# Kernel optimization log

Hardware: AMD Instinct MI355X
Metric: run time of the kernel (lower is better)

## Reference

```python
import jax, jax.numpy as jnp
import numpy as np

IN_C, HID, OUT = 3, 128, 256
K1, K2 = 16, 8
N = 8192


def _knn_idx(x, k):
    # x: [N, C] -> indices of k nearest neighbors (excluding self), [N, k]
    n = x.shape[0]
    sq = jnp.sum(x * x, axis=1)
    d = sq[:, None] + sq[None, :] - 2.0 * (x @ x.T)  # [N, N] squared dists
    i = jnp.arange(n)
    d = d.at[i, i].set(jnp.inf)  # loop=False: exclude self
    _, idx = jax.lax.top_k(-d, k)
    return idx


def _edge_conv(x, W1, b1, W2, b2, k):
    # DynamicEdgeConv: knn graph on x, edge feat [x_i, x_j - x_i], MLP, max aggr
    n, c = x.shape
    idx = _knn_idx(x, k)              # [N, k]
    xj = x[idx]                       # [N, k, C]
    xi = x[:, None, :]                # [N, 1, C]
    e = jnp.concatenate([jnp.broadcast_to(xi, (n, k, c)), xj - xi], axis=-1)  # [N, k, 2C]
    h = jax.nn.relu(e @ W1 + b1) @ W2 + b2  # [N, k, H]
    return jnp.max(h, axis=1)               # max aggregation -> [N, H]


def setup_inputs() -> dict:
    key = jax.random.key(0)
    ks = jax.random.split(key, 9)
    def lin(k, fan_in, fan_out):
        bound = 1.0 / np.sqrt(fan_in)
        kw, kb = jax.random.split(k)
        W = jax.random.uniform(kw, (fan_in, fan_out), jnp.float32, -bound, bound)
        b = jax.random.uniform(kb, (fan_out,), jnp.float32, -bound, bound)
        return W, b
    x = jax.random.normal(ks[0], (N, IN_C), jnp.float32)
    W1a, b1a = lin(ks[1], 2 * IN_C, HID)
    W1b, b1b = lin(ks[2], HID, HID)
    W2a, b2a = lin(ks[3], 2 * HID, OUT)
    W2b, b2b = lin(ks[4], OUT, OUT)
    return {"x": x, "W1a": W1a, "b1a": b1a, "W1b": W1b, "b1b": b1b,
            "W2a": W2a, "b2a": b2a, "W2b": W2b, "b2b": b2b}


def reference(x, W1a, b1a, W1b, b1b, W2a, b2a, W2b, b2b):
    h = _edge_conv(x, W1a, b1a, W1b, b1b, K1)   # [N, HID]
    out = _edge_conv(h, W2a, b2a, W2b, b2b, K2)  # [N, OUT]
    return out
```

## Files before the change

kernel.cpp:

```cpp
#include <hip/hip_runtime.h>
#include <math.h>

constexpr int NPTS  = 8192;
constexpr int HIDC  = 128;
constexpr int OUTC2 = 256;
constexpr int PQC   = 512;
constexpr int KK1   = 16;
constexpr int KK2   = 8;

typedef __attribute__((ext_vector_type(8))) short short8;
typedef __attribute__((ext_vector_type(4))) float f32x4;

__device__ __forceinline__ f32x4 mfma16(short8 a, short8 b, f32x4 c) {
  return __builtin_amdgcn_mfma_f32_16x16x32_bf16(a, b, c, 0, 0, 0);
}

__device__ __forceinline__ void async_ld16(void* lds, const void* g) {
  __builtin_amdgcn_global_load_lds(
      (const __attribute__((address_space(1))) unsigned int*)g,
      (__attribute__((address_space(3))) unsigned int*)lds, 16, 0, 0);
}

template <int K>
__device__ __forceinline__ void ins_u(unsigned (&kk)[K], unsigned v) {
  if (v < kk[K - 1]) {
    kk[K - 1] = v;
    #pragma unroll
    for (int p = K - 1; p > 0; --p) {
      unsigned a = kk[p - 1], b = kk[p];
      kk[p - 1] = a < b ? a : b;
      kk[p]     = a < b ? b : a;
    }
  }
}

template <int K>
__device__ __forceinline__ void ins_lex(float (&kf)[K], int (&ki)[K], float v, int j) {
  bool ins = (v < kf[K - 1]) || (v == kf[K - 1] && j < ki[K - 1]);
  if (ins) {
    kf[K - 1] = v; ki[K - 1] = j;
    #pragma unroll
    for (int p = K - 1; p > 0; --p) {
      float fa = kf[p - 1], fb = kf[p];
      int   ia = ki[p - 1], ib = ki[p];
      bool sw = (fb < fa) || (fb == fa && ib < ia);
      kf[p - 1] = sw ? fb : fa; ki[p - 1] = sw ? ib : ia;
      kf[p]     = sw ? fa : fb; ki[p]     = sw ? ia : ib;
    }
  }
}

__device__ __forceinline__ unsigned short bf16_rn(float x) {
  unsigned int u = __float_as_uint(x);
  unsigned int r = u + 0x7fffu + ((u >> 16) & 1u);
  return (unsigned short)(r >> 16);
}

__global__ void pack_x_kernel(const float* __restrict__ x, float4* __restrict__ x4) {
  int i = blockIdx.x * blockDim.x + threadIdx.x;
  if (i < NPTS) {
    float a = x[3 * i], b = x[3 * i + 1], c = x[3 * i + 2];
    x4[i] = make_float4(a, b, c, a * a + b * b + c * c);
  }
}

__global__ void prep_w1f_kernel(const float* __restrict__ W1,
                                unsigned short* __restrict__ WcFhi,
                                unsigned short* __restrict__ WcFlo) {
  int idx = blockIdx.x * 256 + threadIdx.x;
  int k = idx >> 9, c = idx & 511;
  float wh = W1[(size_t)(HIDC + k) * OUTC2 + (c & 255)];
  float w = (c < OUTC2) ? (W1[(size_t)k * OUTC2 + c] - wh) : wh;
  unsigned short hi = bf16_rn(w);
  float fh = __uint_as_float(((unsigned int)hi) << 16);
  unsigned short lo = bf16_rn(w - fh);
  const int nt = c >> 4, ct = c & 15;
  const int s = k >> 5, kg = (k >> 3) & 3, e = k & 7;
  const size_t fidx = ((size_t)(s * 32 + nt) * 64 + (kg * 16 + ct)) * 8 + e;
  WcFhi[fidx] = hi;
  WcFlo[fidx] = lo;
}

__global__ void prep_w1b_kernel(const float* __restrict__ W,
                                unsigned short* __restrict__ Fhi,
                                unsigned short* __restrict__ Flo) {
  const int c = blockIdx.x;
  const int k = threadIdx.x;
  float w = W[(size_t)k * HIDC + c];
  unsigned short hi = bf16_rn(w);
  float fh = __uint_as_float(((unsigned int)hi) << 16);
  unsigned short lo = bf16_rn(w - fh);
  const int nt = c >> 4, ct = c & 15;
  const int s = k >> 5, kg = (k >> 3) & 3, e = k & 7;
  const size_t idx = ((size_t)(s * 8 + nt) * 64 + (kg * 16 + ct)) * 8 + e;
  Fhi[idx] = hi;
  Flo[idx] = lo;
}

__global__ void prep_w2_kernel(const float* __restrict__ W2,
                               unsigned short* __restrict__ W2Fhi,
                               unsigned short* __restrict__ W2Flo) {
  const int c = blockIdx.x;
  const int k = threadIdx.x;
  float w = W2[(size_t)k * OUTC2 + c];
  unsigned short hi = bf16_rn(w);
  float fh = __uint_as_float(((unsigned int)hi) << 16);
  unsigned short lo = bf16_rn(w - fh);
  const int nt = c >> 4, ct = c & 15;
  const int s  = k >> 5, kg = (k >> 3) & 3, e = k & 7;
  const int lane = kg * 16 + ct;
  const size_t idx = ((size_t)(s * 16 + nt) * 64 + lane) * 8 + e;
  W2Fhi[idx] = hi;
  W2Flo[idx] = lo;
}

__global__ __launch_bounds__(256) void knn3_kernel(const float4* __restrict__ X4,
                                                   int* __restrict__ idx_out) {
  const int tid  = threadIdx.x;
  const int lane = tid & 63;
  const int wv   = __builtin_amdgcn_readfirstlane(tid >> 6);
  const int q    = blockIdx.x * 4 + wv;

  const float4 qv = X4[q];

  unsigned kk[KK2];
  #pragma unroll
  for (int k = 0; k < KK2; ++k) kk[k] = 0xFFFFFFFFu;

  for (int c = 0; c < NPTS / 64; ++c) {
    const int j = c * 64 + lane;
    float4 pj = X4[j];
    float d = fmaxf(qv.w + pj.w - 2.f * (qv.x * pj.x + qv.y * pj.y + qv.z * pj.z), 0.f);
    unsigned key = (__float_as_uint(d) & 0xFFFFE000u) | (unsigned)j;
    if (j == q) key = 0xFFFFFFFFu;
    ins_u<KK2>(kk, key);
  }

  float kf[KK2]; int kj[KK2];
  #pragma unroll
  for (int k = 0; k < KK2; ++k) { kf[k] = INFINITY; kj[k] = 0x7fffffff; }
  #pragma unroll
  for (int k = 0; k < KK2; ++k) {
    int j = (int)(kk[k] & 0x1FFFu);
    float4 pj = X4[j];
    float d = qv.w + pj.w - 2.f * (qv.x * pj.x + qv.y * pj.y + qv.z * pj.z);
    if (kk[k] == 0xFFFFFFFFu) { d = INFINITY; j = 0x7fffffff; }
    ins_lex<KK2>(kf, kj, d, j);
  }

  #pragma unroll
  for (int k = 0; k < KK1; ++k) {
    float mf = kf[0]; int mj = kj[0];
    #pragma unroll
    for (int m = 1; m <= 32; m <<= 1) {
      float of = __shfl_xor(mf, m, 64);
      int   oj = __shfl_xor(mj, m, 64);
      bool g = (of < mf) || (of == mf && oj < mj);
      mf = g ? of : mf; mj = g ? oj : mj;
    }
    const bool won = (kf[0] == mf) && (kj[0] == mj);
    if (won) {
      idx_out[(size_t)q * KK1 + k] = mj;
      #pragma unroll
      for (int p = 0; p < KK2 - 1; ++p) { kf[p] = kf[p + 1]; kj[p] = kj[p + 1]; }
      kf[KK2 - 1] = INFINITY; kj[KK2 - 1] = 0x7fffffff;
    }
  }
}

__global__ __launch_bounds__(512) void edgeconv1_kernel(
    const float* __restrict__ X, const int* __restrict__ knn,
    const float* __restrict__ W1, const float* __restrict__ b1,
    const unsigned short* __restrict__ W1bFhi, const unsigned short* __restrict__ W1bFlo,
    const float* __restrict__ b2,
    float* __restrict__ H, unsigned short* __restrict__ Hhi,
    unsigned short* __restrict__ Hlo, float* __restrict__ SQ2) {
  __shared__ __align__(16) unsigned short Ghi[128 * HIDC];
  __shared__ __align__(16) unsigned short Glo[128 * HIDC];
  __shared__ __align__(16) unsigned short Bs[2][2][4096];
  __shared__ float xjs[8][KK1][3];
  __shared__ float xis[8][3];
  const int tid  = threadIdx.x;
  const int lane = tid & 63;
  const int wv   = __builtin_amdgcn_readfirstlane(tid >> 6);
  const int p    = blockIdx.x * 8 + wv;

  if (lane < KK1) {
    int j = knn[p * KK1 + lane];
    xjs[wv][lane][0] = X[3 * j]; xjs[wv][lane][1] = X[3 * j + 1]; xjs[wv][lane][2] = X[3 * j + 2];
  } else if (lane < KK1 + 3) {
    xis[wv][lane - KK1] = X[3 * p + lane - KK1];
  }
  __syncthreads();

  {
    const int ch0 = lane * 2;
    float2 w1r[6];
    #pragma unroll
    for (int c = 0; c < 6; ++c)
      w1r[c] = make_float2(W1[c * HIDC + ch0], W1[c * HIDC + ch0 + 1]);
    const float2 b1v = make_float2(b1[ch0], b1[ch0 + 1]);
    const float xi0 = xis[wv][0], xi1 = xis[wv][1], xi2 = xis[wv][2];
    const float base0 = b1v.x + xi0 * w1r[0].x + xi1 * w1r[1].x + xi2 * w1r[2].x;
    const float base1 = b1v.y + xi0 * w1r[0].y + xi1 * w1r[1].y + xi2 * w1r[2].y;
    #pragma unroll
    for (int e = 0; e < KK1; ++e) {
      float dx = xjs[wv][e][0] - xi0, dy = xjs[wv][e][1] - xi1, dz = xjs[wv][e][2] - xi2;
      float v0 = fmaxf(base0 + dx * w1r[3].x + dy * w1r[4].x + dz * w1r[5].x, 0.f);
      float v1 = fmaxf(base1 + dx * w1r[3].y + dy * w1r[4].y + dz * w1r[5].y, 0.f);
      unsigned short h0 = bf16_rn(v0), h1s = bf16_rn(v1);
      unsigned short l0 = bf16_rn(v0 - __uint_as_float(((unsigned)h0) << 16));
      unsigned short l1 = bf16_rn(v1 - __uint_as_float(((unsigned)h1s) << 16));
      const int r   = wv * 16 + e;
      const int off = r * 256 + (((ch0 >> 3) ^ (r & 7)) << 4) + ((ch0 & 7) << 1);
      *(ushort2*)((char*)Ghi + off) = make_ushort2(h0, h1s);
      *(ushort2*)((char*)Glo + off) = make_ushort2(l0, l1);
    }
  }

  auto stageB = [&](int buf, int s) {
    const size_t go = (size_t)s * 4096 + (size_t)wv * 512 + (size_t)lane * 8;
    async_ld16((char*)&Bs[buf][0][0] + wv * 1024, W1bFhi + go);
    async_ld16((char*)&Bs[buf][1][0] + wv * 1024, W1bFlo + go);
  };

  stageB(0, 0);
  asm volatile("s_waitcnt vmcnt(0)" ::: "memory");
  __syncthreads();

  const int col = lane & 15;
  const int kg  = lane >> 4;
  const int ar  = wv * 16 + col;
  const int abase = ar * 256;

  f32x4 acc[8];
  #pragma unroll
  for (int n = 0; n < 8; ++n) acc[n] = (f32x4){0.f, 0.f, 0.f, 0.f};

  for (int s = 0; s < 4; ++s) {
    const int cur = s & 1;
    if (s + 1 < 4) stageB(cur ^ 1, s + 1);
    const int asl = (((s * 4 + kg) ^ (ar & 7)) << 4);
    short8 ghi = *(const short8*)((const char*)Ghi + abase + asl);
    short8 glo = *(const short8*)((const char*)Glo + abase + asl);
    #pragma unroll
    for (int n = 0; n < 8; ++n) {
      const int bo = (n * 64 + lane) * 16;
      short8 bhi = *(const short8*)((const char*)&Bs[cur][0][0] + bo);
      short8 blo = *(const short8*)((const char*)&Bs[cur][1][0] + bo);
      acc[n] = mfma16(ghi, bhi, acc[n]);
      acc[n] = mfma16(ghi, blo, acc[n]);
      acc[n] = mfma16(glo, bhi, acc[n]);
    }
    asm volatile("s_waitcnt vmcnt(0)" ::: "memory");
    __syncthreads();
  }

  float sq = 0.f;
  float hv[8];
  #pragma unroll
  for (int n = 0; n < 8; ++n) {
    float m = fmaxf(fmaxf(acc[n][0], acc[n][1]), fmaxf(acc[n][2], acc[n][3]));
    m = fmaxf(m, __shfl_xor(m, 16, 64));
    m = fmaxf(m, __shfl_xor(m, 32, 64));
    m += b2[n * 16 + col];
    hv[n] = m;
    sq += m * m;
  }
  if (kg == 0) {
    #pragma unroll
    for (int n = 0; n < 8; ++n) {
      const int ch = n * 16 + col;
      H[(size_t)p * HIDC + ch] = hv[n];
      unsigned short hb = bf16_rn(hv[n]);
      float fh = __uint_as_float(((unsigned)hb) << 16);
      Hhi[(size_t)p * HIDC + ch] = hb;
      Hlo[(size_t)p * HIDC + ch] = bf16_rn(hv[n] - fh);
    }
  }
  #pragma unroll
  for (int m2 = 1; m2 <= 8; m2 <<= 1) sq += __shfl_xor(sq, m2, 64);
  if (lane == 0) SQ2[p] = sq;
}

__global__ __launch_bounds__(512) void gemm_pq_kernel(
    const unsigned short* __restrict__ Hhi, const unsigned short* __restrict__ Hlo,
    const unsigned short* __restrict__ WcFhi, const unsigned short* __restrict__ WcFlo,
    const float* __restrict__ b1, float* __restrict__ PQ) {
  __shared__ __align__(16) unsigned short Ahi[64 * HIDC];
  __shared__ __align__(16) unsigned short Alo[64 * HIDC];
  __shared__ __align__(16) unsigned short Bsl[2][2][8192];
  const int tid  = threadIdx.x;
  const int lane = tid & 63;
  const int wv   = __builtin_amdgcn_readfirstlane(tid >> 6);
  const int mb   = blockIdx.x >> 1;
  const int ns   = blockIdx.x & 1;
  const int r0   = mb * 64;

  #pragma unroll
  for (int i = 0; i < 2; ++i) {
    const int srow = wv * 8 + i * 4 + (lane >> 4);
    const int sslt = (lane & 15) ^ (srow & 7);
    const size_t go = (size_t)(r0 + srow) * HIDC + sslt * 8;
    async_ld16((char*)Ahi + (wv * 8 + i * 4) * 256, Hhi + go);
    async_ld16((char*)Alo + (wv * 8 + i * 4) * 256, Hlo + go);
  }
  auto stageB = [&](int buf, int s) {
    #pragma unroll
    for (int i = 0; i < 2; ++i) {
      const size_t go = (size_t)(s * 32 + ns * 16) * 512 + (size_t)wv * 1024 + i * 512 + lane * 8;
      async_ld16((char*)&Bsl[buf][0][0] + wv * 2048 + i * 1024, WcFhi + go);
      async_ld16((char*)&Bsl[buf][1][0] + wv * 2048 + i * 1024, WcFlo + go);
    }
  };
  stageB(0, 0);
  asm volatile("s_waitcnt vmcnt(0)" ::: "memory");
  __syncthreads();

  const int col = lane & 15;
  const int kg  = lane >> 4;
  const int mt  = wv & 3;
  const int nh  = wv >> 2;
  const int ar  = mt * 16 + col;
  const int abase = ar * 256;

  f32x4 acc[8];
  #pragma unroll
  for (int n = 0; n < 8; ++n) acc[n] = (f32x4){0.f, 0.f, 0.f, 0.f};

  for (int s = 0; s < 4; ++s) {
    const int cur = s & 1;
    if (s + 1 < 4) stageB(cur ^ 1, s + 1);
    const int asl = (((s * 4 + kg) ^ (ar & 7)) << 4);
    short8 ahi8 = *(const short8*)((const char*)Ahi + abase + asl);
    short8 alo8 = *(const short8*)((const char*)Alo + abase + asl);
    #pragma unroll
    for (int n = 0; n < 8; ++n) {
      const int ntl = nh * 8 + n;
      const int bo = (ntl * 64 + lane) * 16;
      short8 bhi = *(const short8*)((const char*)&Bsl[cur][0][0] + bo);
      short8 blo = *(const short8*)((const char*)&Bsl[cur][1][0] + bo);
      acc[n] = mfma16(ahi8, bhi, acc[n]);
      acc[n] = mfma16(ahi8, blo, acc[n]);
      acc[n] = mfma16(alo8, bhi, acc[n]);
    }
    asm volatile("s_waitcnt vmcnt(0)" ::: "memory");
    __syncthreads();
  }

  #pragma unroll
  for (int n = 0; n < 8; ++n) {
    const int cg = ns * 256 + (nh * 8 + n) * 16 + col;
    const float bb = (ns == 0) ? b1[cg] : 0.f;
    #pragma unroll
    for (int r = 0; r < 4; ++r) {
      const int row = r0 + mt * 16 + kg * 4 + r;
      PQ[(size_t)row * PQC + cg] = acc[n][r] + bb;
    }
  }
}

constexpr int JSPLIT = 16;
constexpr int JPB2   = NPTS / JSPLIT;
constexpr int NCH    = JPB2 / 16;
constexpr int CPQ    = JSPLIT * KK2;

__global__ __launch_bounds__(256) void knn128_filter_kernel(
    const unsigned short* __restrict__ Hhi, const unsigned short* __restrict__ Hlo,
    const float* __restrict__ SQ, unsigned* __restrict__ pk2) {
  __shared__ __align__(16) unsigned short As[2][2][16 * HIDC];
  const int tid  = threadIdx.x;
  const int lane = tid & 63;
  const int wv   = __builtin_amdgcn_readfirstlane(tid >> 6);
  const int qb   = blockIdx.x >> 4;
  const int js   = blockIdx.x & 15;
  const int col  = lane & 15;
  const int kg   = lane >> 4;
  const int qg   = qb * 64 + wv * 16 + col;

  short8 qhi[4], qlo[4];
  #pragma unroll
  for (int s = 0; s < 4; ++s) {
    const size_t o = (size_t)qg * HIDC + s * 32 + kg * 8;
    qhi[s] = *reinterpret_cast<const short8*>(Hhi + o);
    qlo[s] = *reinterpret_cast<const short8*>(Hlo + o);
  }
  const float sqq = SQ[qg];

  unsigned kk[KK2];
  #pragma unroll
  for (int k = 0; k < KK2; ++k) kk[k] = 0xFFFFFFFFu;

  const int jbase = js * JPB2;

  const int srow = 4 * wv + (lane >> 4);
  const int sslt = (lane & 15) ^ (srow & 7);
  auto stage = [&](int buf, int ch) {
    const size_t gofs = (size_t)(jbase + ch * 16 + srow) * HIDC + sslt * 8;
    async_ld16((char*)&As[buf][0][0] + wv * 1024, Hhi + gofs);
    async_ld16((char*)&As[buf][1][0] + wv * 1024, Hlo + gofs);
  };

  stage(0, 0);
  asm volatile("s_waitcnt vmcnt(0)" ::: "memory");
  __syncthreads();

  for (int ch = 0; ch < NCH; ++ch) {
    const int cur = ch & 1;
    if (ch + 1 < NCH) stage(cur ^ 1, ch + 1);

    const int jb = jbase + ch * 16;
    short8 ahi[4], alo[4];
    const int rowb = col * 256;
    #pragma unroll
    for (int s = 0; s < 4; ++s) {
      const int sl = ((s * 4 + kg) ^ (col & 7)) * 16;
      ahi[s] = *(const short8*)((const char*)&As[cur][0][0] + rowb + sl);
      alo[s] = *(const short8*)((const char*)&As[cur][1][0] + rowb + sl);
    }
    f32x4 sqjv = *reinterpret_cast<const f32x4*>(SQ + jb + kg * 4);

    f32x4 acc = {0.f, 0.f, 0.f, 0.f};
    #pragma unroll
    for (int s = 0; s < 4; ++s) {
      acc = mfma16(ahi[s], qhi[s], acc);
      acc = mfma16(ahi[s], qlo[s], acc);
      acc = mfma16(alo[s], qhi[s], acc);
    }
    #pragma unroll
    for (int r = 0; r < 4; ++r) {
      const int jg = jb + kg * 4 + r;
      float d = fmaxf(sqq + sqjv[r] - 2.f * acc[r], 0.f);
      unsigned key = (__float_as_uint(d) & 0xFFFFE000u) | (unsigned)jg;
      if (jg == qg) key = 0xFFFFFFFFu;
      ins_u<KK2>(kk, key);
    }
    asm volatile("s_waitcnt vmcnt(0)" ::: "memory");
    __syncthreads();
  }

  #pragma unroll
  for (int dlt = 16; dlt <= 32; dlt <<= 1) {
    unsigned ok[KK2];
    #pragma unroll
    for (int k = 0; k < KK2; ++k) ok[k] = __shfl_xor((int)kk[k], dlt, 64);
    #pragma unroll
    for (int k = 0; k < KK2; ++k) ins_u<KK2>(kk, ok[k]);
  }
  if (lane < 16) {
    const size_t base = (size_t)qg * CPQ + js * KK2;
    #pragma unroll
    for (int k = 0; k < KK2; ++k) pk2[base + k] = kk[k];
  }
}

__global__ __launch_bounds__(256) void knn_rescore_kernel(
    const float* __restrict__ H, const float* __restrict__ SQ,
    const unsigned* __restrict__ pk2, int* __restrict__ idx_out) {
  __shared__ float qrow[16][HIDC + 4];
  const int tid  = threadIdx.x;
  const int lane = tid & 63;
  const int wv   = tid >> 6;
  const int g    = lane >> 4;
  const int sl   = lane & 15;
  const int q0   = blockIdx.x * 16;
  const int qloc = wv * 4 + g;
  const int q    = q0 + qloc;

  for (int u = tid; u < 16 * 32; u += 256) {
    int r = u >> 5, c4 = u & 31;
    *(f32x4*)&qrow[r][c4 * 4] = *(const f32x4*)&H[(size_t)(q0 + r) * HIDC + c4 * 4];
  }
  __syncthreads();

  unsigned kreg[KK2];
  {
    const unsigned* src = pk2 + (size_t)q * CPQ + sl * KK2;
    uint4 a = *(const uint4*)(src);
    uint4 b = *(const uint4*)(src + 4);
    kreg[0] = a.x; kreg[1] = a.y; kreg[2] = a.z; kreg[3] = a.w;
    kreg[4] = b.x; kreg[5] = b.y; kreg[6] = b.z; kreg[7] = b.w;
  }

  unsigned ckey = 0xFFFFFFFFu;
  #pragma unroll
  for (int t = 0; t < 16; ++t) {
    unsigned m = kreg[0];
    #pragma unroll
    for (int mm = 1; mm <= 8; mm <<= 1) {
      unsigned o = (unsigned)__shfl_xor((int)m, mm, 64);
      m = o < m ? o : m;
    }
    if (t == sl) ckey = m;
    const bool won = (kreg[0] == m);
    if (won) {
      #pragma unroll
      for (int p = 0; p < KK2 - 1; ++p) kreg[p] = kreg[p + 1];
      kreg[KK2 - 1] = 0xFFFFFFFFu;
    }
  }
  const int ci = (int)(ckey & 0x1FFFu);

  const float* crow = H + (size_t)ci * HIDC;
  float dot = 0.f;
  #pragma unroll 8
  for (int c4 = 0; c4 < HIDC / 4; ++c4) {
    f32x4 qv = *(const f32x4*)&qrow[qloc][c4 * 4];
    f32x4 cv = *(const f32x4*)(crow + c4 * 4);
    dot += qv[0] * cv[0] + qv[1] * cv[1] + qv[2] * cv[2] + qv[3] * cv[3];
  }
  float d = SQ[q] + SQ[ci] - 2.f * dot;

  float kf[KK2]; int ki[KK2];
  kf[0] = d; ki[0] = ci;
  #pragma unroll
  for (int k = 1; k < KK2; ++k) { kf[k] = INFINITY; ki[k] = 0x7fffffff; }
  #pragma unroll
  for (int dlt = 1; dlt <= 8; dlt <<= 1) {
    float of[KK2]; int oi[KK2];
    #pragma unroll
    for (int k = 0; k < KK2; ++k) { of[k] = __shfl_xor(kf[k], dlt, 64); oi[k] = __shfl_xor(ki[k], dlt, 64); }
    #pragma unroll
    for (int k = 0; k < KK2; ++k) ins_lex<KK2>(kf, ki, of[k], oi[k]);
  }
  if (sl == 0) {
    #pragma unroll
    for (int k = 0; k < KK2; ++k) idx_out[(size_t)q * KK2 + k] = ki[k];
  }
}

__global__ __launch_bounds__(512) void edgeconv2_kernel(
    const float* __restrict__ PQ, const int* __restrict__ knn,
    const unsigned short* __restrict__ W2Fhi, const unsigned short* __restrict__ W2Flo,
    const float* __restrict__ b2, float* __restrict__ Out) {
  __shared__ __align__(16) unsigned short Ghi[64 * OUTC2];
  __shared__ __align__(16) unsigned short Glo[64 * OUTC2];
  __shared__ __align__(16) unsigned short Bs[2][2][8192];
  const int tid  = threadIdx.x;
  const int lane = tid & 63;
  const int wv   = __builtin_amdgcn_readfirstlane(tid >> 6);
  const int p_base = blockIdx.x * 8;

  {
    const int p   = p_base + wv;
    const int ch0 = lane * 4;
    f32x4 pv = *(const f32x4*)&PQ[(size_t)p * PQC + ch0];
    #pragma unroll
    for (int e = 0; e < KK2; ++e) {
      const int j = knn[p * KK2 + e];
      f32x4 qv = *(const f32x4*)&PQ[(size_t)j * PQC + OUTC2 + ch0];
      unsigned short hb[4], lb[4];
      #pragma unroll
      for (int c = 0; c < 4; ++c) {
        float g = fmaxf(pv[c] + qv[c], 0.f);
        hb[c] = bf16_rn(g);
        float fh = __uint_as_float(((unsigned int)hb[c]) << 16);
        lb[c] = bf16_rn(g - fh);
      }
      const int r   = wv * 8 + e;
      const int off = r * 512 + (((ch0 >> 3) ^ (r & 7)) << 4) + ((ch0 & 7) << 1);
      *(ushort4*)((char*)Ghi + off) = make_ushort4(hb[0], hb[1], hb[2], hb[3]);
      *(ushort4*)((char*)Glo + off) = make_ushort4(lb[0], lb[1], lb[2], lb[3]);
    }
  }

  auto stageB = [&](int buf, int s) {
    #pragma unroll
    for (int i = 0; i < 2; ++i) {
      const size_t go = (size_t)s * 8192 + (size_t)(wv * 2 + i) * 512 + (size_t)lane * 8;
      async_ld16((char*)&Bs[buf][0][0] + (wv * 2 + i) * 1024, W2Fhi + go);
      async_ld16((char*)&Bs[buf][1][0] + (wv * 2 + i) * 1024, W2Flo + go);
    }
  };

  stageB(0, 0);
  asm volatile("s_waitcnt vmcnt(0)" ::: "memory");
  __syncthreads();

  const int col = lane & 15;
  const int kg  = lane >> 4;
  const int mt  = wv & 3;
  const int nh  = wv >> 2;
  const int ar  = mt * 16 + col;
  const int abase = ar * 512;

  f32x4 acc[8];
  #pragma unroll
  for (int n = 0; n < 8; ++n) acc[n] = (f32x4){0.f, 0.f, 0.f, 0.f};

  for (int s = 0; s < 8; ++s) {
    const int cur = s & 1;
    if (s + 1 < 8) stageB(cur ^ 1, s + 1);

    const int asl = (((s * 4 + kg) ^ (ar & 7)) << 4);
    short8 ghi = *(const short8*)((const char*)Ghi + abase + asl);
    short8 glo = *(const short8*)((const char*)Glo + abase + asl);
    #pragma unroll
    for (int n = 0; n < 8; ++n) {
      const int nt = nh * 8 + n;
      const int bo = (nt * 64 + lane) * 16;
      short8 bhi = *(const short8*)((const char*)&Bs[cur][0][0] + bo);
      short8 blo = *(const short8*)((const char*)&Bs[cur][1][0] + bo);
      acc[n] = mfma16(ghi, bhi, acc[n]);
      acc[n] = mfma16(ghi, blo, acc[n]);
      acc[n] = mfma16(glo, bhi, acc[n]);
    }
    asm volatile("s_waitcnt vmcnt(0)" ::: "memory");
    __syncthreads();
  }

  const int pt = p_base + mt * 2 + (kg >> 1);
  #pragma unroll
  for (int n = 0; n < 8; ++n) {
    float m = fmaxf(fmaxf(acc[n][0], acc[n][1]), fmaxf(acc[n][2], acc[n][3]));
    m = fmaxf(m, __shfl_xor(m, 16, 64));
    if ((kg & 1) == 0) {
      const int ncol = nh * 128 + n * 16 + col;
      Out[(size_t)pt * OUTC2 + ncol] = m + b2[ncol];
    }
  }
}

extern "C" void kernel_launch(void* const* d_in, const int* in_sizes, int n_in,
                              void* d_out, int out_size, void* d_ws, size_t ws_size,
                              hipStream_t stream) {
  const float* x   = (const float*)d_in[0];
  const float* W1a = (const float*)d_in[1];
  const float* b1a = (const float*)d_in[2];
  const float* W1b = (const float*)d_in[3];
  const float* b1b = (const float*)d_in[4];
  const float* W2a = (const float*)d_in[5];
  const float* b2a = (const float*)d_in[6];
  const float* W2b = (const float*)d_in[7];
  const float* b2b = (const float*)d_in[8];
  float* out = (float*)d_out;

  float* h    = (float*)d_ws;
  float* sq2  = h + (size_t)NPTS * HIDC;
  int*   idx1 = (int*)(sq2 + NPTS);
  int*   idx2 = idx1 + (size_t)NPTS * KK1;
  unsigned short* Hhi = (unsigned short*)(idx2 + (size_t)NPTS * KK2);
  unsigned short* Hlo = Hhi + (size_t)NPTS * HIDC;
  unsigned* pk2 = (unsigned*)(Hlo + (size_t)NPTS * HIDC);
  float* PQ   = (float*)(pk2 + (size_t)NPTS * CPQ);
  unsigned short* W2Fhi = (unsigned short*)(PQ + (size_t)NPTS * PQC);
  unsigned short* W2Flo = W2Fhi + (size_t)OUTC2 * OUTC2;
  unsigned short* WcFhi = W2Flo + (size_t)OUTC2 * OUTC2;
  unsigned short* WcFlo = WcFhi + (size_t)HIDC * PQC;
  unsigned short* W1bFhi = WcFlo + (size_t)HIDC * PQC;
  unsigned short* W1bFlo = W1bFhi + (size_t)HIDC * HIDC;
  float4* x4 = (float4*)h;

  pack_x_kernel<<<(NPTS + 255) / 256, 256, 0, stream>>>(x, x4);
  prep_w1f_kernel<<<(HIDC * PQC) / 256, 256, 0, stream>>>(W2a, WcFhi, WcFlo);
  prep_w1b_kernel<<<HIDC, HIDC, 0, stream>>>(W1b, W1bFhi, W1bFlo);
  prep_w2_kernel<<<OUTC2, OUTC2, 0, stream>>>(W2b, W2Fhi, W2Flo);
  knn3_kernel<<<NPTS / 4, 256, 0, stream>>>(x4, idx1);
  edgeconv1_kernel<<<NPTS / 8, 512, 0, stream>>>(x, idx1, W1a, b1a,
                                                 W1bFhi, W1bFlo, b1b,
                                                 h, Hhi, Hlo, sq2);
  gemm_pq_kernel<<<(NPTS / 64) * 2, 512, 0, stream>>>(Hhi, Hlo, WcFhi, WcFlo, b2a, PQ);
  knn128_filter_kernel<<<(NPTS / 64) * JSPLIT, 256, 0, stream>>>(Hhi, Hlo, sq2, pk2);
  knn_rescore_kernel<<<NPTS / 16, 256, 0, stream>>>(h, sq2, pk2, idx2);
  edgeconv2_kernel<<<NPTS / 8, 512, 0, stream>>>(PQ, idx2, W2Fhi, W2Flo, b2b, out);
}
```

Measured before the change: 269.1 us.

## Batch top-k insertion with a bitonic merge and process two queries per wave

Replaces the one-at-a-time sorted insertion into the per-lane top-8 list with a merge step: four candidate keys are sorted by a small network and merged into the list with a bitonic half-cleaner, guarded by an early-reject test. The 3-D kNN kernel now handles two queries per wave and loads four points per lane per iteration, reusing each point load across both queries and halving the grid. The aim is fewer serial compare-swap chains and fewer global loads per query, at the cost of more live registers, which could lower occupancy. The filter kernel and its cross-lane merge also use the batched merge.

After: 263.1 us. 1.02x faster.

```diff
diff --git a/kernel.cpp b/kernel.cpp
--- a/kernel.cpp
+++ b/kernel.cpp
@@ -21,16 +21,20 @@
       (__attribute__((address_space(3))) unsigned int*)lds, 16, 0, 0);
 }
 
-template <int K>
-__device__ __forceinline__ void ins_u(unsigned (&kk)[K], unsigned v) {
-  if (v < kk[K - 1]) {
-    kk[K - 1] = v;
-    #pragma unroll
-    for (int p = K - 1; p > 0; --p) {
-      unsigned a = kk[p - 1], b = kk[p];
-      kk[p - 1] = a < b ? a : b;
-      kk[p]     = a < b ? b : a;
-    }
+#define CEU(a, b) { unsigned _t = (a) < (b) ? (a) : (b); (b) = (a) < (b) ? (b) : (a); (a) = _t; }
+
+__device__ __forceinline__ void topk8_batch4(unsigned (&kk)[KK2],
+                                             unsigned b0, unsigned b1,
+                                             unsigned b2, unsigned b3) {
+  CEU(b0, b1); CEU(b2, b3); CEU(b0, b2); CEU(b1, b3); CEU(b1, b2);
+  if (b0 < kk[7]) {
+    kk[4] = kk[4] < b3 ? kk[4] : b3;
+    kk[5] = kk[5] < b2 ? kk[5] : b2;
+    kk[6] = kk[6] < b1 ? kk[6] : b1;
+    kk[7] = kk[7] < b0 ? kk[7] : b0;
+    CEU(kk[0], kk[4]); CEU(kk[1], kk[5]); CEU(kk[2], kk[6]); CEU(kk[3], kk[7]);
+    CEU(kk[0], kk[2]); CEU(kk[1], kk[3]); CEU(kk[4], kk[6]); CEU(kk[5], kk[7]);
+    CEU(kk[0], kk[1]); CEU(kk[2], kk[3]); CEU(kk[4], kk[5]); CEU(kk[6], kk[7]);
   }
 }
 
@@ -119,38 +123,62 @@
   const int tid  = threadIdx.x;
   const int lane = tid & 63;
   const int wv   = __builtin_amdgcn_readfirstlane(tid >> 6);
-  const int q    = blockIdx.x * 4 + wv;
-
-  const float4 qv = X4[q];
-
-  unsigned kk[KK2];
-  #pragma unroll
-  for (int k = 0; k < KK2; ++k) kk[k] = 0xFFFFFFFFu;
-
-  for (int c = 0; c < NPTS / 64; ++c) {
-    const int j = c * 64 + lane;
+  const int qA   = blockIdx.x * 8 + wv * 2;
+  const int qB   = qA + 1;
+
+  const float4 qa = X4[qA];
+  const float4 qb = X4[qB];
+
+  unsigned kkA[KK2], kkB[KK2];
+  #pragma unroll
+  for (int k = 0; k < KK2; ++k) { kkA[k] = 0xFFFFFFFFu; kkB[k] = 0xFFFFFFFFu; }
+
+  for (int c = 0; c < NPTS / 256; ++c) {
+    const int j = c * 256 + lane * 4;
+    float4 p[4];
+    #pragma unroll
+    for (int t = 0; t < 4; ++t) p[t] = X4[j + t];
+
+    unsigned ka[4], kb[4];
+    #pragma unroll
+    for (int t = 0; t < 4; ++t) {
+      float dA = fmaxf(qa.w + p[t].w - 2.f * (qa.x * p[t].x + qa.y * p[t].y + qa.z * p[t].z), 0.f);
+      float dB = fmaxf(qb.w + p[t].w - 2.f * (qb.x * p[t].x + qb.y * p[t].y + qb.z * p[t].z), 0.f);
+      ka[t] = (__float_as_uint(dA) & 0xFFFFE000u) | (unsigned)(j + t);
+      kb[t] = (__float_as_uint(dB) & 0xFFFFE000u) | (unsigned)(j + t);
+      if (j + t == qA) ka[t] = 0xFFFFFFFFu;
+      if (j + t == qB) kb[t] = 0xFFFFFFFFu;
+    }
+    topk8_batch4(kkA, ka[0], ka[1], ka[2], ka[3]);
+    topk8_batch4(kkB, kb[0], kb[1], kb[2], kb[3]);
+  }
+
+  float kfA[KK2], kfB[KK2]; int kjA[KK2], kjB[KK2];
+  #pragma unroll
+  for (int k = 0; k < KK2; ++k) {
+    kfA[k] = INFINITY; kjA[k] = 0x7fffffff;
+    kfB[k] = INFINITY; kjB[k] = 0x7fffffff;
+  }
+  #pragma unroll
+  for (int k = 0; k < KK2; ++k) {
+    int j = (int)(kkA[k] & 0x1FFFu);
     float4 pj = X4[j];
-    float d = fmaxf(qv.w + pj.w - 2.f * (qv.x * pj.x + qv.y * pj.y + qv.z * pj.z), 0.f);
-    unsigned key = (__float_as_uint(d) & 0xFFFFE000u) | (unsigned)j;
-    if (j == q) key = 0xFFFFFFFFu;
-    ins_u<KK2>(kk, key);
-  }
-
-  float kf[KK2]; int kj[KK2];
-  #pragma unroll
-  for (int k = 0; k < KK2; ++k) { kf[k] = INFINITY; kj[k] = 0x7fffffff; }
+    float d = qa.w + pj.w - 2.f * (qa.x * pj.x + qa.y * pj.y + qa.z * pj.z);
+    if (kkA[k] == 0xFFFFFFFFu) { d = INFINITY; j = 0x7fffffff; }
+    ins_lex<KK2>(kfA, kjA, d, j);
+  }
   #pragma unroll
   for (int k = 0; k < KK2; ++k) {
-    int j = (int)(kk[k] & 0x1FFFu);
+    int j = (int)(kkB[k] & 0x1FFFu);
     float4 pj = X4[j];
-    float d = qv.w + pj.w - 2.f * (qv.x * pj.x + qv.y * pj.y + qv.z * pj.z);
-    if (kk[k] == 0xFFFFFFFFu) { d = INFINITY; j = 0x7fffffff; }
-    ins_lex<KK2>(kf, kj, d, j);
+    float d = qb.w + pj.w - 2.f * (qb.x * pj.x + qb.y * pj.y + qb.z * pj.z);
+    if (kkB[k] == 0xFFFFFFFFu) { d = INFINITY; j = 0x7fffffff; }
+    ins_lex<KK2>(kfB, kjB, d, j);
   }
 
   #pragma unroll
   for (int k = 0; k < KK1; ++k) {
-    float mf = kf[0]; int mj = kj[0];
+    float mf = kfA[0]; int mj = kjA[0];
     #pragma unroll
     for (int m = 1; m <= 32; m <<= 1) {
       float of = __shfl_xor(mf, m, 64);
@@ -158,12 +186,30 @@
       bool g = (of < mf) || (of == mf && oj < mj);
       mf = g ? of : mf; mj = g ? oj : mj;
     }
-    const bool won = (kf[0] == mf) && (kj[0] == mj);
+    const bool won = (kfA[0] == mf) && (kjA[0] == mj);
     if (won) {
-      idx_out[(size_t)q * KK1 + k] = mj;
+      idx_out[(size_t)qA * KK1 + k] = mj;
       #pragma unroll
-      for (int p = 0; p < KK2 - 1; ++p) { kf[p] = kf[p + 1]; kj[p] = kj[p + 1]; }
-      kf[KK2 - 1] = INFINITY; kj[KK2 - 1] = 0x7fffffff;
+      for (int p = 0; p < KK2 - 1; ++p) { kfA[p] = kfA[p + 1]; kjA[p] = kjA[p + 1]; }
+      kfA[KK2 - 1] = INFINITY; kjA[KK2 - 1] = 0x7fffffff;
+    }
+  }
+  #pragma unroll
+  for (int k = 0; k < KK1; ++k) {
+    float mf = kfB[0]; int mj = kjB[0];
+    #pragma unroll
+    for (int m = 1; m <= 32; m <<= 1) {
+      float of = __shfl_xor(mf, m, 64);
+      int   oj = __shfl_xor(mj, m, 64);
+      bool g = (of < mf) || (of == mf && oj < mj);
+      mf = g ? of : mf; mj = g ? oj : mj;
+    }
+    const bool won = (kfB[0] == mf) && (kjB[0] == mj);
+    if (won) {
+      idx_out[(size_t)qB * KK1 + k] = mj;
+      #pragma unroll
+      for (int p = 0; p < KK2 - 1; ++p) { kfB[p] = kfB[p + 1]; kjB[p] = kjB[p + 1]; }
+      kfB[KK2 - 1] = INFINITY; kjB[KK2 - 1] = 0x7fffffff;
     }
   }
 }
@@ -427,14 +473,15 @@
       acc = mfma16(ahi[s], qlo[s], acc);
       acc = mfma16(alo[s], qhi[s], acc);
     }
+    unsigned kb[4];
     #pragma unroll
     for (int r = 0; r < 4; ++r) {
       const int jg = jb + kg * 4 + r;
       float d = fmaxf(sqq + sqjv[r] - 2.f * acc[r], 0.f);
-      unsigned key = (__float_as_uint(d) & 0xFFFFE000u) | (unsigned)jg;
-      if (jg == qg) key = 0xFFFFFFFFu;
-      ins_u<KK2>(kk, key);
-    }
+      kb[r] = (__float_as_uint(d) & 0xFFFFE000u) | (unsigned)jg;
+      if (jg == qg) kb[r] = 0xFFFFFFFFu;
+    }
+    topk8_batch4(kk, kb[0], kb[1], kb[2], kb[3]);
     asm volatile("s_waitcnt vmcnt(0)" ::: "memory");
     __syncthreads();
   }
@@ -444,8 +491,8 @@
     unsigned ok[KK2];
     #pragma unroll
     for (int k = 0; k < KK2; ++k) ok[k] = __shfl_xor((int)kk[k], dlt, 64);
-    #pragma unroll
-    for (int k = 0; k < KK2; ++k) ins_u<KK2>(kk, ok[k]);
+    topk8_batch4(kk, ok[0], ok[1], ok[2], ok[3]);
+    topk8_batch4(kk, ok[4], ok[5], ok[6], ok[7]);
   }
   if (lane < 16) {
     const size_t base = (size_t)qg * CPQ + js * KK2;
@@ -655,7 +702,7 @@
   prep_w1f_kernel<<<(HIDC * PQC) / 256, 256, 0, stream>>>(W2a, WcFhi, WcFlo);
   prep_w1b_kernel<<<HIDC, HIDC, 0, stream>>>(W1b, W1bFhi, W1bFlo);
   prep_w2_kernel<<<OUTC2, OUTC2, 0, stream>>>(W2b, W2Fhi, W2Flo);
-  knn3_kernel<<<NPTS / 4, 256, 0, stream>>>(x4, idx1);
+  knn3_kernel<<<NPTS / 8, 256, 0, stream>>>(x4, idx1);
   edgeconv1_kernel<<<NPTS / 8, 512, 0, stream>>>(x, idx1, W1a, b1a,
                                                  W1bFhi, W1bFlo, b1b,
                                                  h, Hhi, Hlo, sq2);
```
